# Performance work log

Measured on AMD Instinct MI355X. Metric: run time of the kernel, lower is better.

The kernel has to match this reference:

```python
import jax, jax.numpy as jnp
import numpy as np

DIM = 512
CTX = 768
GROUPS = 32
EPS = 1e-5


def setup_inputs() -> dict:
    key = jax.random.key(0)
    ks = jax.random.split(key, 12)
    B, H, W, S = 16, 64, 64, 256
    x = jax.random.normal(ks[0], (B, DIM, H, W), dtype=jnp.float32)
    context = jax.random.normal(ks[1], (B, S, CTX), dtype=jnp.float32)
    gn_w = jnp.ones((DIM,), jnp.float32)
    gn_b = jnp.zeros((DIM,), jnp.float32)
    ln_w = jnp.ones((CTX,), jnp.float32)
    ln_b = jnp.zeros((CTX,), jnp.float32)
    wq = jax.random.normal(ks[2], (DIM, DIM), jnp.float32) * (DIM ** -0.5)
    bq = jnp.zeros((DIM,), jnp.float32)
    wkv = jax.random.normal(ks[3], (2 * DIM, CTX), jnp.float32) * (CTX ** -0.5)
    bkv = jnp.zeros((2 * DIM,), jnp.float32)
    wo = jax.random.normal(ks[4], (DIM, DIM), jnp.float32) * (DIM ** -0.5)
    bo = jnp.zeros((DIM,), jnp.float32)
    return {"x": x, "context": context, "gn_w": gn_w, "gn_b": gn_b,
            "ln_w": ln_w, "ln_b": ln_b, "wq": wq, "bq": bq,
            "wkv": wkv, "bkv": bkv, "wo": wo, "bo": bo}


def reference(x, context, gn_w, gn_b, ln_w, ln_b, wq, bq, wkv, bkv, wo, bo):
    b, c, h, w = x.shape
    scale = c ** -0.5
    # GroupNorm over (channels-per-group, H, W)
    xr = x.reshape(b, GROUPS, -1)
    mu = xr.mean(-1, keepdims=True)
    var = xr.var(-1, keepdims=True)
    xn = ((xr - mu) * jax.lax.rsqrt(var + EPS)).reshape(b, c, h, w)
    xn = xn * gn_w[None, :, None, None] + gn_b[None, :, None, None]
    # 1x1 conv query projection as channel GEMM
    q = jnp.einsum('bchw,oc->bohw', xn, wq) + bq[None, :, None, None]
    q = q.reshape(b, c, h * w).transpose(0, 2, 1)  # b, hw, c
    # LayerNorm on context
    cm = context.mean(-1, keepdims=True)
    cv = context.var(-1, keepdims=True)
    cn = (context - cm) * jax.lax.rsqrt(cv + EPS) * ln_w + ln_b
    kv = cn @ wkv.T + bkv  # b, s, 2c
    k, v = jnp.split(kv, 2, axis=-1)
    sim = jnp.einsum('bic,bjc->bij', q, k) * scale
    attn = jax.nn.softmax(sim, axis=-1)
    out = jnp.einsum('bij,bjc->bic', attn, v)
    out = out.transpose(0, 2, 1).reshape(b, c, h, w)
    out = jnp.einsum('bchw,oc->bohw', out, wo) + bo[None, :, None, None]
    return out + x
```

## Files before the change

### kernel.cpp

```cpp
#include <hip/hip_runtime.h>

typedef unsigned short u16;
typedef __attribute__((ext_vector_type(8))) short short8;
typedef __attribute__((ext_vector_type(4))) float f32x4;

#define DIM 512
#define CTX 768
#define HW 4096
#define NB 16
#define NS 256
#define EPSV 1e-5f

__device__ inline u16 f2bf(float f) {
    union { float f; unsigned u; } x; x.f = f;
    unsigned r = x.u + 0x7fffu + ((x.u >> 16) & 1u);
    return (u16)(r >> 16);
}
__device__ inline float bf2f(u16 v) {
    union { unsigned u; float f; } x; x.u = (unsigned)v << 16; return x.f;
}

__global__ void gn_stats(const float* __restrict__ x, const float* __restrict__ gn_w,
                         const float* __restrict__ gn_b, float* __restrict__ ga,
                         float* __restrict__ gd) {
    const int bg = blockIdx.x;
    const int b = bg >> 5, g = bg & 31;
    const float* base = x + ((long)b * DIM + g * 16) * HW;
    float s1 = 0.f, s2 = 0.f;
    const int tid = threadIdx.x;
    for (int i = tid; i < 16384; i += 256) {
        float4 v = ((const float4*)base)[i];
        s1 += v.x + v.y + v.z + v.w;
        s2 += v.x * v.x + v.y * v.y + v.z * v.z + v.w * v.w;
    }
    __shared__ float r1[256], r2[256];
    r1[tid] = s1; r2[tid] = s2; __syncthreads();
    for (int s = 128; s > 0; s >>= 1) {
        if (tid < s) { r1[tid] += r1[tid + s]; r2[tid] += r2[tid + s]; }
        __syncthreads();
    }
    __shared__ float mu_s, rs_s;
    if (tid == 0) {
        float mu = r1[0] * (1.f / 65536.f);
        float var = r2[0] * (1.f / 65536.f) - mu * mu;
        mu_s = mu; rs_s = rsqrtf(var + EPSV);
    }
    __syncthreads();
    if (tid < 16) {
        int c = g * 16 + tid;
        float aa = rs_s * gn_w[c];
        ga[b * DIM + c] = aa;
        gd[b * DIM + c] = gn_b[c] - mu_s * aa;
    }
}

__global__ void gn_apply_t(const float* __restrict__ x, const float* __restrict__ ga,
                           const float* __restrict__ gd, u16* __restrict__ xnt) {
    const int b = blockIdx.y;
    const int c0 = (blockIdx.x & 15) * 32;
    const int p0 = (blockIdx.x >> 4) * 32;
    const int tx = threadIdx.x & 31, ty = threadIdx.x >> 5;
    __shared__ u16 tile[32][33];
    #pragma unroll
    for (int i = 0; i < 4; i++) {
        int c = c0 + ty + i * 8;
        float v = x[((long)b * DIM + c) * HW + p0 + tx];
        v = v * ga[b * DIM + c] + gd[b * DIM + c];
        tile[ty + i * 8][tx] = f2bf(v);
    }
    __syncthreads();
    #pragma unroll
    for (int i = 0; i < 4; i++) {
        int p = p0 + ty + i * 8;
        xnt[((long)b * HW + p) * DIM + c0 + tx] = tile[tx][ty + i * 8];
    }
}

__global__ void ln_ctx(const float* __restrict__ ctx, const float* __restrict__ ln_w,
                       const float* __restrict__ ln_b, u16* __restrict__ cn) {
    const int row = blockIdx.x;
    const int tid = threadIdx.x;
    const float* r = ctx + (long)row * CTX;
    float v[3]; float s1 = 0.f, s2 = 0.f;
    #pragma unroll
    for (int i = 0; i < 3; i++) { v[i] = r[tid + i * 256]; s1 += v[i]; s2 += v[i] * v[i]; }
    __shared__ float r1[256], r2[256];
    r1[tid] = s1; r2[tid] = s2; __syncthreads();
    for (int s = 128; s > 0; s >>= 1) {
        if (tid < s) { r1[tid] += r1[tid + s]; r2[tid] += r2[tid + s]; }
        __syncthreads();
    }
    __shared__ float mu_s, rs_s;
    if (tid == 0) {
        float mu = r1[0] * (1.f / 768.f);
        float var = r2[0] * (1.f / 768.f) - mu * mu;
        mu_s = mu; rs_s = rsqrtf(var + EPSV);
    }
    __syncthreads();
    #pragma unroll
    for (int i = 0; i < 3; i++) {
        int idx = tid + i * 256;
        cn[(long)row * CTX + idx] = f2bf((v[i] - mu_s) * rs_s * ln_w[idx] + ln_b[idx]);
    }
}

__global__ void cvt_weights(const float* __restrict__ wq, const float* __restrict__ wkv,
                            const float* __restrict__ wo, u16* __restrict__ wqtb,
                            u16* __restrict__ wkvb, u16* __restrict__ wob) {
    int i = blockIdx.x * 256 + threadIdx.x;
    if (i < 262144) {
        wqtb[(i & 511) * 512 + (i >> 9)] = f2bf(wq[i]);
        wob[i] = f2bf(wo[i]);
    }
    if (i < 786432) wkvb[i] = f2bf(wkv[i]);
}

__global__ void kbias_k(const u16* __restrict__ k, const float* __restrict__ bq,
                        float* __restrict__ kbias) {
    const int row = blockIdx.x;
    const int tid = threadIdx.x;
    const u16* r = k + (long)row * DIM;
    float s = bf2f(r[tid]) * bq[tid] + bf2f(r[tid + 256]) * bq[tid + 256];
    __shared__ float red[256];
    red[tid] = s; __syncthreads();
    for (int st = 128; st > 0; st >>= 1) {
        if (tid < st) red[tid] += red[tid + st];
        __syncthreads();
    }
    if (tid == 0) kbias[row] = red[0];
}

template <int EPI>
__launch_bounds__(256, 2)
__global__ void gemm_nt(const u16* __restrict__ A, const u16* __restrict__ Bm,
                        const float* __restrict__ bias, const float* __restrict__ xres,
                        void* __restrict__ out0, void* __restrict__ out1,
                        int M, int N, int K, long batchA, long batchB,
                        long obatch, int ldo) {
    __shared__ __align__(16) char smem_raw[2 * 128 * 56 * 2];
    u16 (*As)[56] = (u16(*)[56])smem_raw;
    u16 (*Bs)[56] = (u16(*)[56])(smem_raw + 128 * 56 * 2);
    const int tid = threadIdx.x;
    const int lane = tid & 63;
    const int wave = tid >> 6;
    const int bb = blockIdx.y;
    const int tiles_n = N >> 7;
    const int m0 = (blockIdx.x / tiles_n) << 7;
    const int n0 = (blockIdx.x % tiles_n) << 7;
    const u16* Ab = A + (long)bb * batchA + (long)m0 * K;
    const u16* Bb = Bm + (long)bb * batchB + (long)n0 * K;

    const int sr = tid >> 2;
    const int sc = (tid & 3) << 3;
    const int l16 = lane & 15;
    const int quad = lane >> 4;
    const int wr = (wave >> 1) << 6;
    const int wc = (wave & 1) << 6;

    f32x4 acc[4][4] = {};

    for (int k0 = 0; k0 < K; k0 += 32) {
        __syncthreads();
        *(short8*)&As[sr][sc]      = *(const short8*)(Ab + (long)sr * K + k0 + sc);
        *(short8*)&As[sr + 64][sc] = *(const short8*)(Ab + (long)(sr + 64) * K + k0 + sc);
        *(short8*)&Bs[sr][sc]      = *(const short8*)(Bb + (long)sr * K + k0 + sc);
        *(short8*)&Bs[sr + 64][sc] = *(const short8*)(Bb + (long)(sr + 64) * K + k0 + sc);
        __syncthreads();
        short8 af[4], bfr[4];
        #pragma unroll
        for (int i = 0; i < 4; i++) af[i] = *(const short8*)&As[wr + i * 16 + l16][quad * 8];
        #pragma unroll
        for (int j = 0; j < 4; j++) bfr[j] = *(const short8*)&Bs[wc + j * 16 + l16][quad * 8];
        #pragma unroll
        for (int i = 0; i < 4; i++)
            #pragma unroll
            for (int j = 0; j < 4; j++)
                acc[i][j] = __builtin_amdgcn_mfma_f32_16x16x32_bf16(af[i], bfr[j], acc[i][j], 0, 0, 0);
    }

    if (EPI == 6) {
        float* lbuf = (float*)smem_raw;
        #pragma unroll
        for (int t = 0; t < 4; t++) {
            __syncthreads();
            const int tw = (t >= 2) ? 64 : 0;
            if (wc == tw) {
                const int j0 = (t & 1) * 2;
                #pragma unroll
                for (int jj = 0; jj < 2; jj++) {
                    const int j = j0 + jj;
                    const int cl = (wc + j * 16 + l16) - t * 32;
                    #pragma unroll
                    for (int i = 0; i < 4; i++)
                        #pragma unroll
                        for (int r = 0; r < 4; r++)
                            lbuf[cl * 129 + wr + i * 16 + quad * 4 + r] = acc[i][j][r];
                }
            }
            __syncthreads();
            const int p4 = (tid & 31) * 4;
            #pragma unroll
            for (int cc = 0; cc < 4; cc++) {
                const int cl = (tid >> 5) + cc * 8;
                const int cg = n0 + t * 32 + cl;
                float v0 = lbuf[cl * 129 + p4];
                float v1 = lbuf[cl * 129 + p4 + 1];
                float v2 = lbuf[cl * 129 + p4 + 2];
                float v3 = lbuf[cl * 129 + p4 + 3];
                const long idx = (long)bb * obatch + (long)cg * ldo + m0 + p4;
                float4 xr = *(const float4*)&xres[idx];
                const float bv = bias[cg];
                float4 ov;
                ov.x = v0 + xr.x + bv; ov.y = v1 + xr.y + bv;
                ov.z = v2 + xr.z + bv; ov.w = v3 + xr.w + bv;
                *(float4*)&((float*)out0)[idx] = ov;
            }
        }
        return;
    }

    #pragma unroll
    for (int i = 0; i < 4; i++) {
        #pragma unroll
        for (int r = 0; r < 4; r++) {
            const int row = m0 + wr + i * 16 + quad * 4 + r;
            #pragma unroll
            for (int j = 0; j < 4; j++) {
                const int col = n0 + wc + j * 16 + l16;
                float v = acc[i][j][r];
                if (EPI == 0) {
                    v += bias[col];
                    if (col < DIM) ((u16*)out0)[(long)bb * obatch + (long)row * ldo + col] = f2bf(v);
                    else           ((u16*)out1)[(long)bb * obatch + (long)row * ldo + (col - DIM)] = f2bf(v);
                } else if (EPI == 2) {
                    v = (v + bias[bb * NS + col]) * 0.04419417382415922f;
                    ((float*)out0)[(long)bb * obatch + (long)row * ldo + col] = v;
                } else if (EPI == 3) {
                    ((u16*)out0)[(long)bb * obatch + (long)row * ldo + col] = f2bf(v);
                } else {
                    ((u16*)out0)[(long)bb * obatch + (long)col * ldo + row] = f2bf(v);
                }
            }
        }
    }
}

__global__ void softmax_k(const float* __restrict__ sim, u16* __restrict__ attn) {
    const int row = blockIdx.x * 4 + (threadIdx.x >> 6);
    const int lane = threadIdx.x & 63;
    float4 v = ((const float4*)(sim + (long)row * NS))[lane];
    float m = fmaxf(fmaxf(v.x, v.y), fmaxf(v.z, v.w));
    #pragma unroll
    for (int off = 32; off > 0; off >>= 1) m = fmaxf(m, __shfl_xor(m, off));
    float e0 = __expf(v.x - m), e1 = __expf(v.y - m), e2 = __expf(v.z - m), e3 = __expf(v.w - m);
    float s = e0 + e1 + e2 + e3;
    #pragma unroll
    for (int off = 32; off > 0; off >>= 1) s += __shfl_xor(s, off);
    float inv = 1.f / s;
    unsigned long long pk = (unsigned long long)f2bf(e0 * inv)
                          | ((unsigned long long)f2bf(e1 * inv) << 16)
                          | ((unsigned long long)f2bf(e2 * inv) << 32)
                          | ((unsigned long long)f2bf(e3 * inv) << 48);
    *(unsigned long long*)&attn[(long)row * NS + lane * 4] = pk;
}

extern "C" void kernel_launch(void* const* d_in, const int* in_sizes, int n_in,
                              void* d_out, int out_size, void* d_ws, size_t ws_size,
                              hipStream_t stream) {
    const float* x    = (const float*)d_in[0];
    const float* ctx  = (const float*)d_in[1];
    const float* gn_w = (const float*)d_in[2];
    const float* gn_b = (const float*)d_in[3];
    const float* ln_w = (const float*)d_in[4];
    const float* ln_b = (const float*)d_in[5];
    const float* wq   = (const float*)d_in[6];
    const float* bq   = (const float*)d_in[7];
    const float* wkv  = (const float*)d_in[8];
    const float* bkv  = (const float*)d_in[9];
    const float* wo   = (const float*)d_in[10];
    const float* bo   = (const float*)d_in[11];

    char* ws = (char*)d_ws;
    u16*   xnt  = (u16*)(ws + 0);
    u16*   attn = (u16*)(ws + 67108864);
    u16*   cn   = (u16*)(ws + 100663296);
    u16*   kb_  = (u16*)(ws + 106954752);
    u16*   vb_  = (u16*)(ws + 111149056);
    u16*   Kq   = (u16*)(ws + 115343360);
    u16*   Vot  = (u16*)(ws + 119537664);
    u16*   wqtb = (u16*)(ws + 123731968);
    u16*   wkvb = (u16*)(ws + 124256256);
    u16*   wob  = (u16*)(ws + 125829120);
    float* ga   = (float*)(ws + 126353408);
    float* gd   = ga + NB * DIM;
    float* kbias = (float*)(ws + 126418944);
    float* sim  = (float*)d_out;

    gn_stats<<<dim3(NB * 32), dim3(256), 0, stream>>>(x, gn_w, gn_b, ga, gd);
    gn_apply_t<<<dim3(2048, NB), dim3(256), 0, stream>>>(x, ga, gd, xnt);
    ln_ctx<<<dim3(NB * NS), dim3(256), 0, stream>>>(ctx, ln_w, ln_b, cn);
    cvt_weights<<<dim3(3072), dim3(256), 0, stream>>>(wq, wkv, wo, wqtb, wkvb, wob);

    gemm_nt<0><<<dim3(2 * 8, NB), dim3(256), 0, stream>>>(
        cn, wkvb, bkv, nullptr, kb_, vb_, NS, 2 * DIM, CTX,
        (long)NS * CTX, 0, (long)NS * DIM, DIM);
    gemm_nt<3><<<dim3(2 * 4, NB), dim3(256), 0, stream>>>(
        kb_, wqtb, nullptr, nullptr, Kq, nullptr, NS, DIM, DIM,
        (long)NS * DIM, 0, (long)NS * DIM, DIM);
    kbias_k<<<dim3(NB * NS), dim3(256), 0, stream>>>(kb_, bq, kbias);
    gemm_nt<5><<<dim3(2 * 4, NB), dim3(256), 0, stream>>>(
        vb_, wob, nullptr, nullptr, Vot, nullptr, NS, DIM, DIM,
        (long)NS * DIM, 0, (long)DIM * NS, NS);
    gemm_nt<2><<<dim3(32 * 2, NB), dim3(256), 0, stream>>>(
        xnt, Kq, kbias, nullptr, sim, nullptr, HW, NS, DIM,
        (long)HW * DIM, (long)NS * DIM, (long)HW * NS, NS);
    softmax_k<<<dim3(16384), dim3(256), 0, stream>>>(sim, attn);
    gemm_nt<6><<<dim3(32 * 4, NB), dim3(256), 0, stream>>>(
        attn, Vot, bo, x, d_out, nullptr, HW, DIM, NS,
        (long)HW * NS, (long)DIM * NS, (long)DIM * HW, HW);
}
```

Before: 479.5 us.

## Fuse QK GEMM, softmax and PV/output GEMM into one flash-style attention kernel

Replaces the separate score GEMM, softmax kernel and attention-times-V GEMM with a single kernel. Each block computes a 128-row score tile over all 256 keys in registers, does the softmax with cross-wave reductions in shared memory, stores probabilities in LDS, and multiplies by V tiles with the bias and residual epilogue. This removes the fp32 score and bf16 probability round trips through global memory and two launches. The cost is a very large LDS footprint (one block per CU) and many barriers with no load/compute overlap.

```diff
diff --git a/kernel.cpp b/kernel.cpp
--- a/kernel.cpp
+++ b/kernel.cpp
@@ -133,13 +133,12 @@
 template <int EPI>
 __launch_bounds__(256, 2)
 __global__ void gemm_nt(const u16* __restrict__ A, const u16* __restrict__ Bm,
-                        const float* __restrict__ bias, const float* __restrict__ xres,
+                        const float* __restrict__ bias,
                         void* __restrict__ out0, void* __restrict__ out1,
                         int M, int N, int K, long batchA, long batchB,
                         long obatch, int ldo) {
-    __shared__ __align__(16) char smem_raw[2 * 128 * 56 * 2];
-    u16 (*As)[56] = (u16(*)[56])smem_raw;
-    u16 (*Bs)[56] = (u16(*)[56])(smem_raw + 128 * 56 * 2);
+    __shared__ u16 As[128][56];
+    __shared__ u16 Bs[128][56];
     const int tid = threadIdx.x;
     const int lane = tid & 63;
     const int wave = tid >> 6;
@@ -178,47 +177,6 @@
                 acc[i][j] = __builtin_amdgcn_mfma_f32_16x16x32_bf16(af[i], bfr[j], acc[i][j], 0, 0, 0);
     }
 
-    if (EPI == 6) {
-        float* lbuf = (float*)smem_raw;
-        #pragma unroll
-        for (int t = 0; t < 4; t++) {
-            __syncthreads();
-            const int tw = (t >= 2) ? 64 : 0;
-            if (wc == tw) {
-                const int j0 = (t & 1) * 2;
-                #pragma unroll
-                for (int jj = 0; jj < 2; jj++) {
-                    const int j = j0 + jj;
-                    const int cl = (wc + j * 16 + l16) - t * 32;
-                    #pragma unroll
-                    for (int i = 0; i < 4; i++)
-                        #pragma unroll
-                        for (int r = 0; r < 4; r++)
-                            lbuf[cl * 129 + wr + i * 16 + quad * 4 + r] = acc[i][j][r];
-                }
-            }
-            __syncthreads();
-            const int p4 = (tid & 31) * 4;
-            #pragma unroll
-            for (int cc = 0; cc < 4; cc++) {
-                const int cl = (tid >> 5) + cc * 8;
-                const int cg = n0 + t * 32 + cl;
-                float v0 = lbuf[cl * 129 + p4];
-                float v1 = lbuf[cl * 129 + p4 + 1];
-                float v2 = lbuf[cl * 129 + p4 + 2];
-                float v3 = lbuf[cl * 129 + p4 + 3];
-                const long idx = (long)bb * obatch + (long)cg * ldo + m0 + p4;
-                float4 xr = *(const float4*)&xres[idx];
-                const float bv = bias[cg];
-                float4 ov;
-                ov.x = v0 + xr.x + bv; ov.y = v1 + xr.y + bv;
-                ov.z = v2 + xr.z + bv; ov.w = v3 + xr.w + bv;
-                *(float4*)&((float*)out0)[idx] = ov;
-            }
-        }
-        return;
-    }
-
     #pragma unroll
     for (int i = 0; i < 4; i++) {
         #pragma unroll
@@ -232,9 +190,6 @@
                     v += bias[col];
                     if (col < DIM) ((u16*)out0)[(long)bb * obatch + (long)row * ldo + col] = f2bf(v);
                     else           ((u16*)out1)[(long)bb * obatch + (long)row * ldo + (col - DIM)] = f2bf(v);
-                } else if (EPI == 2) {
-                    v = (v + bias[bb * NS + col]) * 0.04419417382415922f;
-                    ((float*)out0)[(long)bb * obatch + (long)row * ldo + col] = v;
                 } else if (EPI == 3) {
                     ((u16*)out0)[(long)bb * obatch + (long)row * ldo + col] = f2bf(v);
                 } else {
@@ -245,23 +200,181 @@
     }
 }
 
-__global__ void softmax_k(const float* __restrict__ sim, u16* __restrict__ attn) {
-    const int row = blockIdx.x * 4 + (threadIdx.x >> 6);
-    const int lane = threadIdx.x & 63;
-    float4 v = ((const float4*)(sim + (long)row * NS))[lane];
-    float m = fmaxf(fmaxf(v.x, v.y), fmaxf(v.z, v.w));
-    #pragma unroll
-    for (int off = 32; off > 0; off >>= 1) m = fmaxf(m, __shfl_xor(m, off));
-    float e0 = __expf(v.x - m), e1 = __expf(v.y - m), e2 = __expf(v.z - m), e3 = __expf(v.w - m);
-    float s = e0 + e1 + e2 + e3;
-    #pragma unroll
-    for (int off = 32; off > 0; off >>= 1) s += __shfl_xor(s, off);
-    float inv = 1.f / s;
-    unsigned long long pk = (unsigned long long)f2bf(e0 * inv)
-                          | ((unsigned long long)f2bf(e1 * inv) << 16)
-                          | ((unsigned long long)f2bf(e2 * inv) << 32)
-                          | ((unsigned long long)f2bf(e3 * inv) << 48);
-    *(unsigned long long*)&attn[(long)row * NS + lane * 4] = pk;
+__launch_bounds__(512, 2)
+__global__ void flash_attn(const u16* __restrict__ xnt, const u16* __restrict__ Kq,
+                           const u16* __restrict__ Vot, const float* __restrict__ kbias,
+                           const float* __restrict__ bo, const float* __restrict__ x,
+                           float* __restrict__ out) {
+    __shared__ __align__(16) char fsm[153728];
+    u16 (*P)[264]      = (u16(*)[264])(fsm);
+    u16 (*As)[56]      = (u16(*)[56])(fsm + 67584);
+    u16 (*Bs)[56]      = (u16(*)[56])(fsm + 67584 + 128 * 56 * 2);
+    u16 (*Vs)[264]     = (u16(*)[264])(fsm + 67584);
+    float (*red)[4]    = (float(*)[4])(fsm + 135168);
+    float (*lbuf)[129] = (float(*)[129])(fsm + 137216);
+
+    const int tid = threadIdx.x;
+    const int lane = tid & 63;
+    const int wave = tid >> 6;
+    const int mw = wave >> 2;
+    const int nw = wave & 3;
+    const int l16 = lane & 15;
+    const int quad = lane >> 4;
+    const int b = blockIdx.y;
+    const int m0 = blockIdx.x << 7;
+
+    const u16* Ab = xnt + ((long)b * HW + m0) * DIM;
+    const u16* Bb = Kq + (long)b * NS * DIM;
+
+    f32x4 acc[4][4] = {};
+    for (int k0 = 0; k0 < DIM; k0 += 32) {
+        __syncthreads();
+        {
+            const int r = tid >> 2, c = (tid & 3) << 3;
+            *(short8*)&As[r][c] = *(const short8*)(Ab + (long)r * DIM + k0 + c);
+            const int r2 = tid >> 1, c2 = (tid & 1) << 4;
+            *(short8*)&Bs[r2][c2]     = *(const short8*)(Bb + (long)r2 * DIM + k0 + c2);
+            *(short8*)&Bs[r2][c2 + 8] = *(const short8*)(Bb + (long)r2 * DIM + k0 + c2 + 8);
+        }
+        __syncthreads();
+        short8 af[4], bfr[4];
+        #pragma unroll
+        for (int i = 0; i < 4; i++) af[i] = *(const short8*)&As[mw * 64 + i * 16 + l16][quad * 8];
+        #pragma unroll
+        for (int j = 0; j < 4; j++) bfr[j] = *(const short8*)&Bs[nw * 64 + j * 16 + l16][quad * 8];
+        #pragma unroll
+        for (int i = 0; i < 4; i++)
+            #pragma unroll
+            for (int j = 0; j < 4; j++)
+                acc[i][j] = __builtin_amdgcn_mfma_f32_16x16x32_bf16(af[i], bfr[j], acc[i][j], 0, 0, 0);
+    }
+
+    const float scale = 0.044194173824159216f;
+    float kb[4];
+    #pragma unroll
+    for (int j = 0; j < 4; j++) kb[j] = kbias[b * NS + nw * 64 + j * 16 + l16];
+
+    #pragma unroll
+    for (int i = 0; i < 4; i++) {
+        #pragma unroll
+        for (int r = 0; r < 4; r++) {
+            float m = -1e30f;
+            #pragma unroll
+            for (int j = 0; j < 4; j++) {
+                float v = (acc[i][j][r] + kb[j]) * scale;
+                acc[i][j][r] = v;
+                m = fmaxf(m, v);
+            }
+            #pragma unroll
+            for (int off = 1; off < 16; off <<= 1) m = fmaxf(m, __shfl_xor(m, off));
+            if (l16 == 0) red[mw * 64 + i * 16 + quad * 4 + r][nw] = m;
+        }
+    }
+    __syncthreads();
+    float rsum[4][4];
+    #pragma unroll
+    for (int i = 0; i < 4; i++) {
+        #pragma unroll
+        for (int r = 0; r < 4; r++) {
+            const int row = mw * 64 + i * 16 + quad * 4 + r;
+            float4 rv = *(const float4*)red[row];
+            float gm = fmaxf(fmaxf(rv.x, rv.y), fmaxf(rv.z, rv.w));
+            float s = 0.f;
+            #pragma unroll
+            for (int j = 0; j < 4; j++) {
+                float e = __expf(acc[i][j][r] - gm);
+                acc[i][j][r] = e;
+                s += e;
+            }
+            #pragma unroll
+            for (int off = 1; off < 16; off <<= 1) s += __shfl_xor(s, off);
+            rsum[i][r] = s;
+        }
+    }
+    __syncthreads();
+    #pragma unroll
+    for (int i = 0; i < 4; i++)
+        #pragma unroll
+        for (int r = 0; r < 4; r++)
+            if (l16 == 0) red[mw * 64 + i * 16 + quad * 4 + r][nw] = rsum[i][r];
+    __syncthreads();
+    #pragma unroll
+    for (int i = 0; i < 4; i++) {
+        #pragma unroll
+        for (int r = 0; r < 4; r++) {
+            const int row = mw * 64 + i * 16 + quad * 4 + r;
+            float4 sv = *(const float4*)red[row];
+            float inv = 1.f / (sv.x + sv.y + sv.z + sv.w);
+            #pragma unroll
+            for (int j = 0; j < 4; j++)
+                P[row][nw * 64 + j * 16 + l16] = f2bf(acc[i][j][r] * inv);
+        }
+    }
+
+    for (int nc = 0; nc < 4; nc++) {
+        __syncthreads();
+        {
+            const u16* Vb = Vot + ((long)b * DIM + nc * 128) * NS;
+            const int r = tid >> 2, c0 = (tid & 3) << 6;
+            #pragma unroll
+            for (int u = 0; u < 4; u++)
+                *(short8*)&Vs[r][c0 + u * 8] = *(const short8*)(Vb + (long)r * NS + c0 + u * 8);
+            #pragma unroll
+            for (int u = 4; u < 8; u++)
+                *(short8*)&Vs[r][c0 + u * 8] = *(const short8*)(Vb + (long)r * NS + c0 + u * 8);
+        }
+        __syncthreads();
+        f32x4 oacc[4][2];
+        #pragma unroll
+        for (int i = 0; i < 4; i++)
+            #pragma unroll
+            for (int jj = 0; jj < 2; jj++)
+                oacc[i][jj] = (f32x4){0.f, 0.f, 0.f, 0.f};
+        #pragma unroll
+        for (int kk = 0; kk < 8; kk++) {
+            short8 pf[4], vf[2];
+            #pragma unroll
+            for (int i = 0; i < 4; i++)
+                pf[i] = *(const short8*)&P[mw * 64 + i * 16 + l16][kk * 32 + quad * 8];
+            #pragma unroll
+            for (int jj = 0; jj < 2; jj++)
+                vf[jj] = *(const short8*)&Vs[nw * 32 + jj * 16 + l16][kk * 32 + quad * 8];
+            #pragma unroll
+            for (int i = 0; i < 4; i++)
+                #pragma unroll
+                for (int jj = 0; jj < 2; jj++)
+                    oacc[i][jj] = __builtin_amdgcn_mfma_f32_16x16x32_bf16(pf[i], vf[jj], oacc[i][jj], 0, 0, 0);
+        }
+        #pragma unroll
+        for (int t = 0; t < 4; t++) {
+            if (t > 0) __syncthreads();
+            if (nw == t) {
+                #pragma unroll
+                for (int jj = 0; jj < 2; jj++)
+                    #pragma unroll
+                    for (int i = 0; i < 4; i++)
+                        #pragma unroll
+                        for (int r = 0; r < 4; r++)
+                            lbuf[jj * 16 + l16][mw * 64 + i * 16 + quad * 4 + r] = oacc[i][jj][r];
+            }
+            __syncthreads();
+            {
+                const int cl = tid >> 4;
+                const int p8 = (tid & 15) * 8;
+                const int cg = nc * 128 + t * 32 + cl;
+                const long idx = ((long)b * DIM + cg) * HW + m0 + p8;
+                const float bv = bo[cg];
+                float4 v0 = *(const float4*)&lbuf[cl][p8];
+                float4 v1 = *(const float4*)&lbuf[cl][p8 + 4];
+                float4 x0 = *(const float4*)&x[idx];
+                float4 x1 = *(const float4*)&x[idx + 4];
+                v0.x += x0.x + bv; v0.y += x0.y + bv; v0.z += x0.z + bv; v0.w += x0.w + bv;
+                v1.x += x1.x + bv; v1.y += x1.y + bv; v1.z += x1.z + bv; v1.w += x1.w + bv;
+                *(float4*)&out[idx] = v0;
+                *(float4*)&out[idx + 4] = v1;
+            }
+        }
+    }
 }
 
 extern "C" void kernel_launch(void* const* d_in, const int* in_sizes, int n_in,
@@ -282,19 +395,17 @@
 
     char* ws = (char*)d_ws;
     u16*   xnt  = (u16*)(ws + 0);
-    u16*   attn = (u16*)(ws + 67108864);
-    u16*   cn   = (u16*)(ws + 100663296);
-    u16*   kb_  = (u16*)(ws + 106954752);
-    u16*   vb_  = (u16*)(ws + 111149056);
-    u16*   Kq   = (u16*)(ws + 115343360);
-    u16*   Vot  = (u16*)(ws + 119537664);
-    u16*   wqtb = (u16*)(ws + 123731968);
-    u16*   wkvb = (u16*)(ws + 124256256);
-    u16*   wob  = (u16*)(ws + 125829120);
-    float* ga   = (float*)(ws + 126353408);
+    u16*   cn   = (u16*)(ws + 67108864);
+    u16*   kb_  = (u16*)(ws + 73400320);
+    u16*   vb_  = (u16*)(ws + 77594624);
+    u16*   Kq   = (u16*)(ws + 81788928);
+    u16*   Vot  = (u16*)(ws + 85983232);
+    u16*   wqtb = (u16*)(ws + 90177536);
+    u16*   wkvb = (u16*)(ws + 90701824);
+    u16*   wob  = (u16*)(ws + 92274688);
+    float* ga   = (float*)(ws + 92798976);
     float* gd   = ga + NB * DIM;
-    float* kbias = (float*)(ws + 126418944);
-    float* sim  = (float*)d_out;
+    float* kbias = (float*)(ws + 92864512);
 
     gn_stats<<<dim3(NB * 32), dim3(256), 0, stream>>>(x, gn_w, gn_b, ga, gd);
     gn_apply_t<<<dim3(2048, NB), dim3(256), 0, stream>>>(x, ga, gd, xnt);
@@ -302,20 +413,15 @@
     cvt_weights<<<dim3(3072), dim3(256), 0, stream>>>(wq, wkv, wo, wqtb, wkvb, wob);
 
     gemm_nt<0><<<dim3(2 * 8, NB), dim3(256), 0, stream>>>(
-        cn, wkvb, bkv, nullptr, kb_, vb_, NS, 2 * DIM, CTX,
+        cn, wkvb, bkv, kb_, vb_, NS, 2 * DIM, CTX,
         (long)NS * CTX, 0, (long)NS * DIM, DIM);
     gemm_nt<3><<<dim3(2 * 4, NB), dim3(256), 0, stream>>>(
-        kb_, wqtb, nullptr, nullptr, Kq, nullptr, NS, DIM, DIM,
+        kb_, wqtb, nullptr, Kq, nullptr, NS, DIM, DIM,
         (long)NS * DIM, 0, (long)NS * DIM, DIM);
     kbias_k<<<dim3(NB * NS), dim3(256), 0, stream>>>(kb_, bq, kbias);
     gemm_nt<5><<<dim3(2 * 4, NB), dim3(256), 0, stream>>>(
-        vb_, wob, nullptr, nullptr, Vot, nullptr, NS, DIM, DIM,
+        vb_, wob, nullptr, Vot, nullptr, NS, DIM, DIM,
         (long)NS * DIM, 0, (long)DIM * NS, NS);
-    gemm_nt<2><<<dim3(32 * 2, NB), dim3(256), 0, stream>>>(
-        xnt, Kq, kbias, nullptr, sim, nullptr, HW, NS, DIM,
-        (long)HW * DIM, (long)NS * DIM, (long)HW * NS, NS);
-    softmax_k<<<dim3(16384), dim3(256), 0, stream>>>(sim, attn);
-    gemm_nt<6><<<dim3(32 * 4, NB), dim3(256), 0, stream>>>(
-        attn, Vot, bo, x, d_out, nullptr, HW, DIM, NS,
-        (long)HW * NS, (long)DIM * NS, (long)DIM * HW, HW);
-}
+    flash_attn<<<dim3(32, NB), dim3(512), 0, stream>>>(
+        xnt, Kq, Vot, kbias, bo, x, (float*)d_out);
+}
```

Measured after the change: 470.9 us. Within noise of the previous version (-1.8%).
